# Optimization experiments

Measured on AMD Instinct MI355X. Metric: run time of the kernel, lower is better.

Reference implementation:

```python
import jax, jax.numpy as jnp
import numpy as np

BATCH, SEQ, DIM, HEADS, DSTATE, BLOCK = 2, 4096, 1024, 16, 64, 64
LN_EPS = 1e-6

def segsum(x):
    # x: (..., T) -> (..., T, T); segsum[i, j] = sum_{j < k <= i} x[k]; -inf above diagonal
    T = x.shape[-1]
    cs = jnp.cumsum(x, axis=-1)
    seg = cs[..., :, None] - cs[..., None, :]
    mask = jnp.tril(jnp.ones((T, T), dtype=bool))
    return jnp.where(mask, seg, -jnp.inf)

def ssd_minimal_discrete(X, A, C, B, block_len):
    # X: (b,s,h,p) already multiplied by dt; A: (b,s,h) = A*dt; C readout, B input: (b,s,h,n)
    b, s, h, p = X.shape
    n = B.shape[-1]
    c = s // block_len
    l = block_len
    Xc = X.reshape(b, c, l, h, p)
    Bc = B.reshape(b, c, l, h, n)
    Cc = C.reshape(b, c, l, h, n)
    Ac = A.reshape(b, c, l, h).transpose(0, 3, 1, 2)  # (b,h,c,l)
    A_cumsum = jnp.cumsum(Ac, axis=-1)
    # 1. intra-chunk (diagonal block) outputs
    L = jnp.exp(segsum(Ac))  # (b,h,c,l,l)
    Y_diag = jnp.einsum('bclhn,bcshn,bhcls,bcshp->bclhp', Cc, Bc, L, Xc)
    # 2. states at end of each chunk
    decay_states = jnp.exp(A_cumsum[..., -1:] - A_cumsum)
    states = jnp.einsum('bclhn,bhcl,bclhp->bchpn', Bc, decay_states, Xc)
    # 3. inter-chunk recurrence on chunk states
    init = jnp.zeros_like(states[:, :1])
    states = jnp.concatenate([init, states], axis=1)  # (b,c+1,h,p,n)
    decay_chunk = jnp.exp(segsum(jnp.pad(A_cumsum[..., -1], ((0, 0), (0, 0), (1, 0)))))
    new_states = jnp.einsum('bhzc,bchpn->bzhpn', decay_chunk, states)
    states, final_state = new_states[:, :-1], new_states[:, -1]
    # 4. state -> output contribution (off-diagonal blocks)
    state_decay_out = jnp.exp(A_cumsum)
    Y_off = jnp.einsum('bclhn,bchpn,bhcl->bclhp', Cc, states, state_decay_out)
    return (Y_diag + Y_off).reshape(b, s, h, p), final_state

def setup_inputs():
    key = jax.random.key(0)
    ks = jax.random.split(key, 8)
    X = jax.random.normal(ks[0], (BATCH, SEQ, DIM), jnp.float32)
    B = jax.random.normal(ks[1], (BATCH, SEQ, HEADS * DSTATE), jnp.float32)
    C = jax.random.normal(ks[2], (BATCH, SEQ, HEADS * DSTATE), jnp.float32)
    W_dt = jax.random.normal(ks[3], (DIM, HEADS), jnp.float32) * 0.02
    # dt_bias initializer: inverse-softplus of dt ~ LogUniform(1e-3, 1e-1)
    dt = jnp.exp(jax.random.uniform(ks[4], (1, SEQ, HEADS)) * (jnp.log(0.1) - jnp.log(0.001)) + jnp.log(0.001))
    dt = jnp.clip(dt, 1e-4)
    dt_bias = dt + jnp.log(-jnp.expm1(-dt))
    # a_log initializer: log of Uniform(1, 16)
    a_log = jnp.log(jax.random.uniform(ks[5], (HEADS,), minval=1.0, maxval=16.0))
    W_out = jax.random.normal(ks[6], (DIM, DIM), jnp.float32) * 0.02
    ln_scale = jnp.ones((DIM,), jnp.float32)
    ln_bias = jnp.zeros((DIM,), jnp.float32)
    return {"X": X, "B": B, "C": C, "W_dt": W_dt, "dt_bias": dt_bias, "a_log": a_log,
            "W_out": W_out, "ln_scale": ln_scale, "ln_bias": ln_bias, "block_len": BLOCK}

def reference(X, B, C, W_dt, dt_bias, a_log, W_out, ln_scale, ln_bias, block_len):
    b, s, dim = X.shape
    h = a_log.shape[0]
    Xh = X.reshape(b, s, h, -1)
    Bh = B.reshape(b, s, h, -1)
    Ch = C.reshape(b, s, h, -1)
    dt = jax.nn.softplus(jnp.einsum('bsd,dh->bsh', X, W_dt) + dt_bias)  # (b,s,h)
    A = -jnp.exp(a_log)  # (h,)
    y, final_state = ssd_minimal_discrete(Xh * dt[..., None], A * dt, Ch, Bh, block_len)
    y = y.reshape(b, s, dim)
    mu = jnp.mean(y, axis=-1, keepdims=True)
    var = jnp.mean(jnp.square(y - mu), axis=-1, keepdims=True)
    yn = (y - mu) / jnp.sqrt(var + LN_EPS) * ln_scale + ln_bias
    out = jnp.einsum('bsd,de->bse', yn, W_out)
    return out, final_state
```

## Files before the change

### kernel.cpp

```cpp
#include <hip/hip_runtime.h>
#include <hip/hip_bf16.h>
#include <hip/hip_fp16.h>
#include <math.h>

#define BATCH   2
#define SEQ     4096
#define DIM     1024
#define HEADS   16
#define DSTATE  64
#define HEADDIM 64
#define BLOCKL  64
#define NCHUNK  64
#define ROWS    (BATCH*SEQ)

typedef __attribute__((ext_vector_type(4))) float f32x4;
typedef __attribute__((ext_vector_type(8))) short bf16x8;
typedef __attribute__((ext_vector_type(8))) _Float16 f16x8;

static __device__ __forceinline__ float softplus_f(float x){
    return (x > 20.f) ? x : log1pf(__expf(x));
}
static __device__ __forceinline__ ushort f2b(float f){
    __hip_bfloat16 h = __float2bfloat16(f);
    return *reinterpret_cast<ushort*>(&h);
}
static __device__ __forceinline__ float b2f(ushort u){
    uint x = ((uint)u) << 16;
    return *reinterpret_cast<float*>(&x);
}
static __device__ __forceinline__ void gload16(const void* g, void* l){
    __builtin_amdgcn_global_load_lds((const __attribute__((address_space(1))) unsigned int*)g,
                                     (__attribute__((address_space(3))) unsigned int*)l, 16, 0, 0);
}

__global__ __launch_bounds__(256) void k_dt(const float* __restrict__ X,
        const float* __restrict__ Wdt, const float* __restrict__ dtb,
        const float* __restrict__ alog,
        float* __restrict__ dt_g, float* __restrict__ dtA_g){
    int r = blockIdx.x;
    int s = r & (SEQ-1);
    int tid = threadIdx.x;
    __shared__ float xrow[DIM];
    __shared__ float red[16][17];
    *(f32x4*)(xrow + tid*4) = *(const f32x4*)(X + (size_t)r*DIM + tid*4);
    __syncthreads();
    int part = tid >> 4, h = tid & 15;
    int d0 = part * 64;
    float acc = 0.f;
    #pragma unroll 8
    for (int i = 0; i < 64; ++i)
        acc += xrow[d0 + i] * Wdt[(size_t)(d0 + i)*HEADS + h];
    red[part][h] = acc;
    __syncthreads();
    if (tid < 16){
        float sum = 0.f;
        #pragma unroll
        for (int p = 0; p < 16; ++p) sum += red[p][tid];
        sum += dtb[(size_t)s*HEADS + tid];
        float dtv = softplus_f(sum);
        dt_g[(size_t)r*HEADS + tid]  = dtv;
        dtA_g[(size_t)r*HEADS + tid] = -__expf(alog[tid]) * dtv;
    }
}

__global__ __launch_bounds__(256) void k_chunk(const float* __restrict__ X,
        const float* __restrict__ Bin, const float* __restrict__ Cin,
        const float* __restrict__ dt_g, const float* __restrict__ dtA_g,
        ushort* __restrict__ ybf, ushort* __restrict__ cstate, float* __restrict__ css_g){
    int bid = blockIdx.x;
    int h = bid & 15, c = (bid >> 4) & 63, b = bid >> 10;
    int tid = threadIdx.x;
    int lane = tid & 63, wave = tid >> 6;
    int r0 = b*SEQ + c*BLOCKL;

    __shared__ __align__(16) char region0[18432];
    __shared__ __align__(16) ushort XdT[64*72];
    __shared__ __align__(16) ushort WBT[64*72];
    __shared__ float csh[64], dtsh[64], wsh[64];
    ushort* Cs = (ushort*)region0;
    ushort* Bs = (ushort*)(region0 + 9216);
    float*  Mf = (float*)region0;

    int l  = tid >> 2;
    int c0 = (tid & 3) * 16;

    f32x4 xr[4], br[4], cr[4];
    {
        const float* xp = X   + (size_t)(r0 + l)*DIM + h*HEADDIM + c0;
        const float* bp = Bin + (size_t)(r0 + l)*DIM + h*DSTATE  + c0;
        const float* cp = Cin + (size_t)(r0 + l)*DIM + h*DSTATE  + c0;
        #pragma unroll
        for (int q = 0; q < 4; ++q){
            xr[q] = *(const f32x4*)(xp + q*4);
            br[q] = *(const f32x4*)(bp + q*4);
            cr[q] = *(const f32x4*)(cp + q*4);
        }
    }
    if (tid < 64){
        dtsh[tid] = dt_g[(size_t)(r0 + tid)*HEADS + h];
        float a = dtA_g[(size_t)(r0 + tid)*HEADS + h];
        #pragma unroll
        for (int off = 1; off < 64; off <<= 1){
            float v = __shfl_up(a, off, 64);
            if (tid >= off) a += v;
        }
        csh[tid] = a;
        css_g[(size_t)bid*64 + tid] = a;
        float cs63 = __shfl(a, 63, 64);
        wsh[tid] = __expf(cs63 - a);
    }
    ushort tc[16], tb[16];
    #pragma unroll
    for (int q = 0; q < 4; ++q)
        #pragma unroll
        for (int j = 0; j < 4; ++j){
            tc[q*4+j] = f2b(cr[q][j]);
            tb[q*4+j] = f2b(br[q][j]);
        }
    *(uint4*)&Cs[l*72 + c0]     = *(uint4*)&tc[0];
    *(uint4*)&Cs[l*72 + c0 + 8] = *(uint4*)&tc[8];
    *(uint4*)&Bs[l*72 + c0]     = *(uint4*)&tb[0];
    *(uint4*)&Bs[l*72 + c0 + 8] = *(uint4*)&tb[8];
    __syncthreads();

    {
        float dl = dtsh[l], wl = wsh[l];
        #pragma unroll
        for (int q = 0; q < 4; ++q)
            #pragma unroll
            for (int j = 0; j < 4; ++j){
                int p = c0 + q*4 + j;
                XdT[p*72 + l] = f2b(xr[q][j] * dl);
                WBT[p*72 + l] = f2b(br[q][j] * wl);
            }
    }
    __syncthreads();

    int cl15  = lane & 15;
    int g     = lane >> 4;
    int arow  = wave*16 + cl15;
    int kof   = g * 8;
    int rbase = wave*16 + g*4;

    f32x4 gacc[4];
    #pragma unroll
    for (int j = 0; j < 4; ++j) gacc[j] = (f32x4){0.f,0.f,0.f,0.f};
    #pragma unroll
    for (int k = 0; k < 2; ++k){
        bf16x8 a = *(const bf16x8*)&Cs[arow*72 + k*32 + kof];
        #pragma unroll
        for (int j = 0; j < 4; ++j){
            bf16x8 bb = *(const bf16x8*)&Bs[(16*j + cl15)*72 + k*32 + kof];
            gacc[j] = __builtin_amdgcn_mfma_f32_16x16x32_bf16(a, bb, gacc[j], 0, 0, 0);
        }
    }
    __syncthreads();

    #pragma unroll
    for (int j = 0; j < 4; ++j){
        #pragma unroll
        for (int r = 0; r < 4; ++r){
            int row = rbase + r, col = 16*j + cl15;
            float m = 0.f;
            if (col <= row) m = gacc[j][r] * __expf(csh[row] - csh[col]);
            Mf[row*65 + col] = m;
        }
    }
    __syncthreads();

    f32x4 y[4];
    #pragma unroll
    for (int j = 0; j < 4; ++j) y[j] = (f32x4){0.f,0.f,0.f,0.f};
    #pragma unroll
    for (int k = 0; k < 2; ++k){
        bf16x8 am;
        #pragma unroll
        for (int i = 0; i < 8; ++i)
            am[i] = (short)f2b(Mf[arow*65 + k*32 + kof + i]);
        #pragma unroll
        for (int j = 0; j < 4; ++j){
            bf16x8 bx = *(const bf16x8*)&XdT[(16*j + cl15)*72 + k*32 + kof];
            y[j] = __builtin_amdgcn_mfma_f32_16x16x32_bf16(am, bx, y[j], 0, 0, 0);
        }
    }
    #pragma unroll
    for (int j = 0; j < 4; ++j)
        #pragma unroll
        for (int r = 0; r < 4; ++r)
            ybf[(size_t)(r0 + rbase + r)*DIM + h*HEADDIM + 16*j + cl15] = f2b(y[j][r]);

    f32x4 st[4];
    #pragma unroll
    for (int j = 0; j < 4; ++j) st[j] = (f32x4){0.f,0.f,0.f,0.f};
    #pragma unroll
    for (int k = 0; k < 2; ++k){
        bf16x8 aw = *(const bf16x8*)&XdT[arow*72 + k*32 + kof];
        #pragma unroll
        for (int j = 0; j < 4; ++j){
            bf16x8 bb = *(const bf16x8*)&WBT[(16*j + cl15)*72 + k*32 + kof];
            st[j] = __builtin_amdgcn_mfma_f32_16x16x32_bf16(aw, bb, st[j], 0, 0, 0);
        }
    }
    #pragma unroll
    for (int j = 0; j < 4; ++j)
        #pragma unroll
        for (int r = 0; r < 4; ++r){
            __half hv = __float2half(st[j][r]);
            cstate[(size_t)bid*4096 + (size_t)(rbase + r)*64 + 16*j + cl15] = *(ushort*)&hv;
        }
}

__global__ __launch_bounds__(256) void k_scan(ushort* __restrict__ cstate,
        const float* __restrict__ css_g, float* __restrict__ fs_out){
    int bid = blockIdx.x;
    int tile = bid & 7, hh = (bid >> 3) & 15, b = bid >> 7;
    int pn = tile*512 + threadIdx.x*2;
    float P0 = 0.f, P1 = 0.f;
    for (int c = 0; c < NCHUNK; ++c){
        size_t base = (size_t)((b*NCHUNK + c)*HEADS + hh);
        float e = __expf(css_g[base*64 + 63]);
        __half2 cur = *(const __half2*)&cstate[base*4096 + pn];
        *( __half2*)&cstate[base*4096 + pn] = __floats2half2_rn(P0, P1);
        float2 cf = __half22float2(cur);
        P0 = e*P0 + cf.x;
        P1 = e*P1 + cf.y;
    }
    *(float2*)&fs_out[(size_t)(b*HEADS + hh)*4096 + pn] = make_float2(P0, P1);
}

__global__ __launch_bounds__(256) void k_yoff(const float* __restrict__ Cin,
        const ushort* __restrict__ cstate, const float* __restrict__ css_g,
        ushort* __restrict__ ybf){
    int bid = blockIdx.x;
    int h = bid & 15, c = (bid >> 4) & 63, b = bid >> 10;
    int tid = threadIdx.x;
    int lane = tid & 63, wave = tid >> 6;
    int r0 = b*SEQ + c*BLOCKL;
    __shared__ __align__(16) ushort Cs[64*72];
    __shared__ __align__(16) ushort Ss[64*72];
    __shared__ float cse[64];
    {
        int l  = tid >> 2;
        int c0 = (tid & 3) * 16;
        const float* cp = Cin + (size_t)(r0 + l)*DIM + h*DSTATE + c0;
        ushort tc[16];
        #pragma unroll
        for (int q = 0; q < 4; ++q){
            f32x4 vc = *(const f32x4*)(cp + q*4);
            #pragma unroll
            for (int j = 0; j < 4; ++j){
                __half hv = __float2half(vc[j]);
                tc[q*4+j] = *(ushort*)&hv;
            }
        }
        *(uint4*)&Cs[l*72 + c0]     = *(uint4*)&tc[0];
        *(uint4*)&Cs[l*72 + c0 + 8] = *(uint4*)&tc[8];
        const ushort* sp = cstate + (size_t)bid*4096 + (size_t)l*64 + c0;
        *(uint4*)&Ss[l*72 + c0]     = *(const uint4*)sp;
        *(uint4*)&Ss[l*72 + c0 + 8] = *(const uint4*)(sp + 8);
    }
    if (tid < 64) cse[tid] = __expf(css_g[(size_t)bid*64 + tid]);
    __syncthreads();

    int cl15 = lane & 15;
    int g    = lane >> 4;
    int arow = wave*16 + cl15;
    int kof  = g * 8;
    f32x4 acc[4];
    #pragma unroll
    for (int j = 0; j < 4; ++j) acc[j] = (f32x4){0.f,0.f,0.f,0.f};
    #pragma unroll
    for (int k = 0; k < 2; ++k){
        f16x8 a = *(const f16x8*)&Cs[arow*72 + k*32 + kof];
        #pragma unroll
        for (int j = 0; j < 4; ++j){
            f16x8 bb = *(const f16x8*)&Ss[(16*j + cl15)*72 + k*32 + kof];
            acc[j] = __builtin_amdgcn_mfma_f32_16x16x32_f16(a, bb, acc[j], 0, 0, 0);
        }
    }
    int rbase = wave*16 + g*4;
    #pragma unroll
    for (int j = 0; j < 4; ++j)
        #pragma unroll
        for (int r = 0; r < 4; ++r){
            float e = cse[rbase + r];
            size_t idx = (size_t)(r0 + rbase + r)*DIM + h*HEADDIM + 16*j + cl15;
            ybf[idx] = f2b(b2f(ybf[idx]) + e * acc[j][r]);
        }
}

__global__ __launch_bounds__(256) void k_ln(ushort* __restrict__ ybf,
        const float* __restrict__ scale, const float* __restrict__ bias){
    int r = blockIdx.x, tid = threadIdx.x;
    ushort* yp = ybf + (size_t)r*DIM + tid*4;
    short4 raw = *(const short4*)yp;
    float v[4];
    v[0] = b2f((ushort)raw.x); v[1] = b2f((ushort)raw.y);
    v[2] = b2f((ushort)raw.z); v[3] = b2f((ushort)raw.w);
    float s1 = v[0]+v[1]+v[2]+v[3];
    float s2 = v[0]*v[0]+v[1]*v[1]+v[2]*v[2]+v[3]*v[3];
    #pragma unroll
    for (int m = 32; m > 0; m >>= 1){
        s1 += __shfl_xor(s1, m, 64);
        s2 += __shfl_xor(s2, m, 64);
    }
    __shared__ float w1[4], w2[4];
    int wv = tid >> 6;
    if ((tid & 63) == 0){ w1[wv] = s1; w2[wv] = s2; }
    __syncthreads();
    float S1 = w1[0]+w1[1]+w1[2]+w1[3];
    float S2 = w2[0]+w2[1]+w2[2]+w2[3];
    float mu  = S1 * (1.f/DIM);
    float var = S2 * (1.f/DIM) - mu*mu;
    float rstd = rsqrtf(var + 1e-6f);
    int d = tid*4;
    f32x4 sc = *(const f32x4*)(scale + d);
    f32x4 bi = *(const f32x4*)(bias + d);
    ushort o[4];
    #pragma unroll
    for (int j = 0; j < 4; ++j)
        o[j] = f2b((v[j] - mu)*rstd*sc[j] + bi[j]);
    *(short4*)yp = *(short4*)&o[0];
}

__global__ __launch_bounds__(256) void k_wt(const float* __restrict__ W,
        __hip_bfloat16* __restrict__ Wt){
    __shared__ float t[64][65];
    int kt = blockIdx.x >> 4, nt = blockIdx.x & 15;
    int tid = threadIdx.x;
    int lr = tid >> 4, lc4 = (tid & 15) * 4;
    #pragma unroll
    for (int q = 0; q < 4; ++q){
        int k = lr + q*16;
        *(f32x4*)&t[k][lc4] = *(const f32x4*)(W + (size_t)(kt*64 + k)*DIM + nt*64 + lc4);
    }
    __syncthreads();
    #pragma unroll
    for (int q = 0; q < 4; ++q){
        int n = lr + q*16;
        union { __hip_bfloat16 h[4]; short4 s4; } u;
        #pragma unroll
        for (int j = 0; j < 4; ++j) u.h[j] = __float2bfloat16(t[lc4+j][n]);
        *(short4*)((short*)Wt + (size_t)(nt*64 + n)*DIM + kt*64 + lc4) = u.s4;
    }
}

__global__ __launch_bounds__(256) void k_gemm(const __hip_bfloat16* __restrict__ A,
        const __hip_bfloat16* __restrict__ Bt, float* __restrict__ Out){
    __shared__ __align__(16) ushort As[128*32];
    __shared__ __align__(16) ushort Bsh[128*32];
    int bid = blockIdx.x;
    int bn = bid & 7, bm = bid >> 3;
    int tid = threadIdx.x;
    int lane = tid & 63, wave = tid >> 6;
    int wr = wave >> 1, wc = wave & 1;
    f32x4 acc[4][4];
    #pragma unroll
    for (int i = 0; i < 4; ++i)
        #pragma unroll
        for (int j = 0; j < 4; ++j)
            acc[i][j] = (f32x4){0.f, 0.f, 0.f, 0.f};
    const ushort* Ag = (const ushort*)A  + (size_t)bm*128*1024;
    const ushort* Bg = (const ushort*)Bt + (size_t)bn*128*1024;
    int row0 = tid >> 2;
    int col0 = (tid & 3) * 8;
    for (int k0 = 0; k0 < 1024; k0 += 32){
        const ushort* sA = Ag + (size_t)row0*1024 + k0 + col0;
        const ushort* sB = Bg + (size_t)row0*1024 + k0 + col0;
        gload16(sA,           &As[row0*32 + col0]);
        gload16(sA + 64*1024, &As[(row0+64)*32 + col0]);
        gload16(sB,           &Bsh[row0*32 + col0]);
        gload16(sB + 64*1024, &Bsh[(row0+64)*32 + col0]);
        __syncthreads();
        bf16x8 af[4], bfr[4];
        #pragma unroll
        for (int i = 0; i < 4; ++i){
            int arow = wr*64 + i*16 + (lane & 15);
            af[i] = *(const bf16x8*)&As[arow*32 + ((lane >> 4) << 3)];
        }
        #pragma unroll
        for (int j = 0; j < 4; ++j){
            int brow = wc*64 + j*16 + (lane & 15);
            bfr[j] = *(const bf16x8*)&Bsh[brow*32 + ((lane >> 4) << 3)];
        }
        #pragma unroll
        for (int i = 0; i < 4; ++i)
            #pragma unroll
            for (int j = 0; j < 4; ++j)
                acc[i][j] = __builtin_amdgcn_mfma_f32_16x16x32_bf16(af[i], bfr[j], acc[i][j], 0, 0, 0);
        __syncthreads();
    }
    #pragma unroll
    for (int i = 0; i < 4; ++i){
        int m0 = bm*128 + wr*64 + i*16 + ((lane >> 4) << 2);
        #pragma unroll
        for (int j = 0; j < 4; ++j){
            int n = bn*128 + wc*64 + j*16 + (lane & 15);
            #pragma unroll
            for (int reg = 0; reg < 4; ++reg)
                Out[(size_t)(m0 + reg)*1024 + n] = acc[i][j][reg];
        }
    }
}

extern "C" void kernel_launch(void* const* d_in, const int* in_sizes, int n_in,
                              void* d_out, int out_size, void* d_ws, size_t ws_size,
                              hipStream_t stream){
    const float* X    = (const float*)d_in[0];
    const float* Bin  = (const float*)d_in[1];
    const float* Cin  = (const float*)d_in[2];
    const float* Wdt  = (const float*)d_in[3];
    const float* dtb  = (const float*)d_in[4];
    const float* alog = (const float*)d_in[5];
    const float* Wout = (const float*)d_in[6];
    const float* lns  = (const float*)d_in[7];
    const float* lnb  = (const float*)d_in[8];

    float* out = (float*)d_out;
    float* fs_out = out + (size_t)ROWS*DIM;

    float* dt_g   = (float*)d_ws;
    float* dtA_g  = dt_g  + 131072;
    float* css_g  = dtA_g + 131072;
    ushort* cstate = (ushort*)(css_g + 131072);
    ushort* ybf    = cstate + 8388608;
    __hip_bfloat16* Wt = (__hip_bfloat16*)(ybf + 8388608);

    k_dt   <<<ROWS,               256, 0, stream>>>(X, Wdt, dtb, alog, dt_g, dtA_g);
    k_chunk<<<BATCH*NCHUNK*HEADS, 256, 0, stream>>>(X, Bin, Cin, dt_g, dtA_g, ybf, cstate, css_g);
    k_scan <<<BATCH*HEADS*8,      256, 0, stream>>>(cstate, css_g, fs_out);
    k_yoff <<<BATCH*NCHUNK*HEADS, 256, 0, stream>>>(Cin, cstate, css_g, ybf);
    k_ln   <<<ROWS,               256, 0, stream>>>(ybf, lns, lnb);
    k_wt   <<<256,                256, 0, stream>>>(Wout, Wt);
    k_gemm <<<512,                256, 0, stream>>>((const __hip_bfloat16*)ybf, Wt, out);
}
```

Before: 127.0 us.

## Fuse weight transpose into dt kernel, shrink chunk LDS, prefetch scan, remap GEMM blocks

Merges the W_out transpose/bf16 cast into the dt projection kernel as extra blocks, which removes one launch. In the chunk kernel, the masked score matrix is now stored in LDS as bf16 and read with vector loads, and XdT reuses the C/B region, which shrinks LDS use and may allow more resident blocks. The scan prefetches the next chunk state before it is needed. The GEMM block index is remapped so that consecutive blocks share B tiles, for better cache locality. These are several unrelated tweaks, each with a modest expected effect.

```diff
diff --git a/kernel.cpp b/kernel.cpp
--- a/kernel.cpp
+++ b/kernel.cpp
@@ -33,33 +33,56 @@
                                      (__attribute__((address_space(3))) unsigned int*)l, 16, 0, 0);
 }
 
-__global__ __launch_bounds__(256) void k_dt(const float* __restrict__ X,
+__global__ __launch_bounds__(256) void k_dtwt(const float* __restrict__ X,
         const float* __restrict__ Wdt, const float* __restrict__ dtb,
-        const float* __restrict__ alog,
-        float* __restrict__ dt_g, float* __restrict__ dtA_g){
-    int r = blockIdx.x;
-    int s = r & (SEQ-1);
-    int tid = threadIdx.x;
+        const float* __restrict__ alog, const float* __restrict__ W,
+        float* __restrict__ dt_g, float* __restrict__ dtA_g,
+        ushort* __restrict__ Wt){
     __shared__ float xrow[DIM];
     __shared__ float red[16][17];
-    *(f32x4*)(xrow + tid*4) = *(const f32x4*)(X + (size_t)r*DIM + tid*4);
-    __syncthreads();
-    int part = tid >> 4, h = tid & 15;
-    int d0 = part * 64;
-    float acc = 0.f;
-    #pragma unroll 8
-    for (int i = 0; i < 64; ++i)
-        acc += xrow[d0 + i] * Wdt[(size_t)(d0 + i)*HEADS + h];
-    red[part][h] = acc;
-    __syncthreads();
-    if (tid < 16){
-        float sum = 0.f;
-        #pragma unroll
-        for (int p = 0; p < 16; ++p) sum += red[p][tid];
-        sum += dtb[(size_t)s*HEADS + tid];
-        float dtv = softplus_f(sum);
-        dt_g[(size_t)r*HEADS + tid]  = dtv;
-        dtA_g[(size_t)r*HEADS + tid] = -__expf(alog[tid]) * dtv;
+    __shared__ float t[64][65];
+    int bidx = blockIdx.x;
+    int tid = threadIdx.x;
+    if (bidx < ROWS){
+        int r = bidx;
+        int s = r & (SEQ-1);
+        *(f32x4*)(xrow + tid*4) = *(const f32x4*)(X + (size_t)r*DIM + tid*4);
+        __syncthreads();
+        int part = tid >> 4, h = tid & 15;
+        int d0 = part * 64;
+        float acc = 0.f;
+        #pragma unroll 8
+        for (int i = 0; i < 64; ++i)
+            acc += xrow[d0 + i] * Wdt[(size_t)(d0 + i)*HEADS + h];
+        red[part][h] = acc;
+        __syncthreads();
+        if (tid < 16){
+            float sum = 0.f;
+            #pragma unroll
+            for (int p = 0; p < 16; ++p) sum += red[p][tid];
+            sum += dtb[(size_t)s*HEADS + tid];
+            float dtv = softplus_f(sum);
+            dt_g[(size_t)r*HEADS + tid]  = dtv;
+            dtA_g[(size_t)r*HEADS + tid] = -__expf(alog[tid]) * dtv;
+        }
+    } else {
+        int bid = bidx - ROWS;
+        int kt = bid >> 4, nt = bid & 15;
+        int lr = tid >> 4, lc4 = (tid & 15) * 4;
+        #pragma unroll
+        for (int q = 0; q < 4; ++q){
+            int k = lr + q*16;
+            *(f32x4*)&t[k][lc4] = *(const f32x4*)(W + (size_t)(kt*64 + k)*DIM + nt*64 + lc4);
+        }
+        __syncthreads();
+        #pragma unroll
+        for (int q = 0; q < 4; ++q){
+            int n = lr + q*16;
+            ushort o[4];
+            #pragma unroll
+            for (int j = 0; j < 4; ++j) o[j] = f2b(t[lc4+j][n]);
+            *(short4*)(Wt + (size_t)(nt*64 + n)*DIM + kt*64 + lc4) = *(short4*)&o[0];
+        }
     }
 }
 
@@ -74,12 +97,12 @@
     int r0 = b*SEQ + c*BLOCKL;
 
     __shared__ __align__(16) char region0[18432];
-    __shared__ __align__(16) ushort XdT[64*72];
     __shared__ __align__(16) ushort WBT[64*72];
     __shared__ float csh[64], dtsh[64], wsh[64];
-    ushort* Cs = (ushort*)region0;
-    ushort* Bs = (ushort*)(region0 + 9216);
-    float*  Mf = (float*)region0;
+    ushort* Cs  = (ushort*)region0;
+    ushort* Bs  = (ushort*)(region0 + 9216);
+    ushort* Mb  = (ushort*)region0;
+    ushort* XdT = (ushort*)(region0 + 9216);
 
     int l  = tid >> 2;
     int c0 = (tid & 3) * 16;
@@ -109,30 +132,19 @@
         float cs63 = __shfl(a, 63, 64);
         wsh[tid] = __expf(cs63 - a);
     }
-    ushort tc[16], tb[16];
-    #pragma unroll
-    for (int q = 0; q < 4; ++q)
-        #pragma unroll
-        for (int j = 0; j < 4; ++j){
-            tc[q*4+j] = f2b(cr[q][j]);
-            tb[q*4+j] = f2b(br[q][j]);
-        }
-    *(uint4*)&Cs[l*72 + c0]     = *(uint4*)&tc[0];
-    *(uint4*)&Cs[l*72 + c0 + 8] = *(uint4*)&tc[8];
-    *(uint4*)&Bs[l*72 + c0]     = *(uint4*)&tb[0];
-    *(uint4*)&Bs[l*72 + c0 + 8] = *(uint4*)&tb[8];
-    __syncthreads();
-
     {
-        float dl = dtsh[l], wl = wsh[l];
+        ushort tc[16], tb[16];
         #pragma unroll
         for (int q = 0; q < 4; ++q)
             #pragma unroll
             for (int j = 0; j < 4; ++j){
-                int p = c0 + q*4 + j;
-                XdT[p*72 + l] = f2b(xr[q][j] * dl);
-                WBT[p*72 + l] = f2b(br[q][j] * wl);
+                tc[q*4+j] = f2b(cr[q][j]);
+                tb[q*4+j] = f2b(br[q][j]);
             }
+        *(uint4*)&Cs[l*72 + c0]     = *(uint4*)&tc[0];
+        *(uint4*)&Cs[l*72 + c0 + 8] = *(uint4*)&tc[8];
+        *(uint4*)&Bs[l*72 + c0]     = *(uint4*)&tb[0];
+        *(uint4*)&Bs[l*72 + c0 + 8] = *(uint4*)&tb[8];
     }
     __syncthreads();
 
@@ -142,6 +154,14 @@
     int kof   = g * 8;
     int rbase = wave*16 + g*4;
 
+    {
+        float wl = wsh[l];
+        #pragma unroll
+        for (int q = 0; q < 4; ++q)
+            #pragma unroll
+            for (int j = 0; j < 4; ++j)
+                WBT[(c0 + q*4 + j)*72 + l] = f2b(br[q][j] * wl);
+    }
     f32x4 gacc[4];
     #pragma unroll
     for (int j = 0; j < 4; ++j) gacc[j] = (f32x4){0.f,0.f,0.f,0.f};
@@ -163,8 +183,16 @@
             int row = rbase + r, col = 16*j + cl15;
             float m = 0.f;
             if (col <= row) m = gacc[j][r] * __expf(csh[row] - csh[col]);
-            Mf[row*65 + col] = m;
-        }
+            Mb[row*72 + col] = f2b(m);
+        }
+    }
+    {
+        float dl = dtsh[l];
+        #pragma unroll
+        for (int q = 0; q < 4; ++q)
+            #pragma unroll
+            for (int j = 0; j < 4; ++j)
+                XdT[(c0 + q*4 + j)*72 + l] = f2b(xr[q][j] * dl);
     }
     __syncthreads();
 
@@ -173,10 +201,7 @@
     for (int j = 0; j < 4; ++j) y[j] = (f32x4){0.f,0.f,0.f,0.f};
     #pragma unroll
     for (int k = 0; k < 2; ++k){
-        bf16x8 am;
-        #pragma unroll
-        for (int i = 0; i < 8; ++i)
-            am[i] = (short)f2b(Mf[arow*65 + k*32 + kof + i]);
+        bf16x8 am = *(const bf16x8*)&Mb[arow*72 + k*32 + kof];
         #pragma unroll
         for (int j = 0; j < 4; ++j){
             bf16x8 bx = *(const bf16x8*)&XdT[(16*j + cl15)*72 + k*32 + kof];
@@ -215,15 +240,19 @@
     int bid = blockIdx.x;
     int tile = bid & 7, hh = (bid >> 3) & 15, b = bid >> 7;
     int pn = tile*512 + threadIdx.x*2;
+    size_t base0 = (size_t)(b*NCHUNK)*HEADS + hh;
     float P0 = 0.f, P1 = 0.f;
+    __half2 cur = *(const __half2*)&cstate[base0*4096 + pn];
     for (int c = 0; c < NCHUNK; ++c){
-        size_t base = (size_t)((b*NCHUNK + c)*HEADS + hh);
+        size_t base = base0 + (size_t)c*HEADS;
+        __half2 nxt = cur;
+        if (c < NCHUNK-1) nxt = *(const __half2*)&cstate[(base + HEADS)*4096 + pn];
         float e = __expf(css_g[base*64 + 63]);
-        __half2 cur = *(const __half2*)&cstate[base*4096 + pn];
         *( __half2*)&cstate[base*4096 + pn] = __floats2half2_rn(P0, P1);
         float2 cf = __half22float2(cur);
         P0 = e*P0 + cf.x;
         P1 = e*P1 + cf.y;
+        cur = nxt;
     }
     *(float2*)&fs_out[(size_t)(b*HEADS + hh)*4096 + pn] = make_float2(P0, P1);
 }
@@ -323,34 +352,13 @@
     *(short4*)yp = *(short4*)&o[0];
 }
 
-__global__ __launch_bounds__(256) void k_wt(const float* __restrict__ W,
-        __hip_bfloat16* __restrict__ Wt){
-    __shared__ float t[64][65];
-    int kt = blockIdx.x >> 4, nt = blockIdx.x & 15;
-    int tid = threadIdx.x;
-    int lr = tid >> 4, lc4 = (tid & 15) * 4;
-    #pragma unroll
-    for (int q = 0; q < 4; ++q){
-        int k = lr + q*16;
-        *(f32x4*)&t[k][lc4] = *(const f32x4*)(W + (size_t)(kt*64 + k)*DIM + nt*64 + lc4);
-    }
-    __syncthreads();
-    #pragma unroll
-    for (int q = 0; q < 4; ++q){
-        int n = lr + q*16;
-        union { __hip_bfloat16 h[4]; short4 s4; } u;
-        #pragma unroll
-        for (int j = 0; j < 4; ++j) u.h[j] = __float2bfloat16(t[lc4+j][n]);
-        *(short4*)((short*)Wt + (size_t)(nt*64 + n)*DIM + kt*64 + lc4) = u.s4;
-    }
-}
-
-__global__ __launch_bounds__(256) void k_gemm(const __hip_bfloat16* __restrict__ A,
-        const __hip_bfloat16* __restrict__ Bt, float* __restrict__ Out){
+__global__ __launch_bounds__(256) void k_gemm(const ushort* __restrict__ A,
+        const ushort* __restrict__ Bt, float* __restrict__ Out){
     __shared__ __align__(16) ushort As[128*32];
     __shared__ __align__(16) ushort Bsh[128*32];
     int bid = blockIdx.x;
-    int bn = bid & 7, bm = bid >> 3;
+    int wgid = (bid & 7)*64 + (bid >> 3);
+    int bn = wgid & 7, bm = wgid >> 3;
     int tid = threadIdx.x;
     int lane = tid & 63, wave = tid >> 6;
     int wr = wave >> 1, wc = wave & 1;
@@ -360,8 +368,8 @@
         #pragma unroll
         for (int j = 0; j < 4; ++j)
             acc[i][j] = (f32x4){0.f, 0.f, 0.f, 0.f};
-    const ushort* Ag = (const ushort*)A  + (size_t)bm*128*1024;
-    const ushort* Bg = (const ushort*)Bt + (size_t)bn*128*1024;
+    const ushort* Ag = A  + (size_t)bm*128*1024;
+    const ushort* Bg = Bt + (size_t)bn*128*1024;
     int row0 = tid >> 2;
     int col0 = (tid & 3) * 8;
     for (int k0 = 0; k0 < 1024; k0 += 32){
@@ -419,18 +427,18 @@
     float* out = (float*)d_out;
     float* fs_out = out + (size_t)ROWS*DIM;
 
-    float* dt_g   = (float*)d_ws;
-    float* dtA_g  = dt_g  + 131072;
-    float* css_g  = dtA_g + 131072;
-    ushort* cstate = (ushort*)(css_g + 131072);
-    ushort* ybf    = cstate + 8388608;
-    __hip_bfloat16* Wt = (__hip_bfloat16*)(ybf + 8388608);
-
-    k_dt   <<<ROWS,               256, 0, stream>>>(X, Wdt, dtb, alog, dt_g, dtA_g);
+    char* ws = (char*)d_ws;
+    float*  dt_g   = (float*)(ws);
+    float*  dtA_g  = (float*)(ws + 524288);
+    float*  css_g  = (float*)(ws + 1048576);
+    ushort* cstate = (ushort*)(ws + 1572864);
+    ushort* ybf    = (ushort*)(ws + 18350080);
+    ushort* Wt     = (ushort*)(ws + 35127296);
+
+    k_dtwt <<<ROWS + 256,         256, 0, stream>>>(X, Wdt, dtb, alog, Wout, dt_g, dtA_g, Wt);
     k_chunk<<<BATCH*NCHUNK*HEADS, 256, 0, stream>>>(X, Bin, Cin, dt_g, dtA_g, ybf, cstate, css_g);
     k_scan <<<BATCH*HEADS*8,      256, 0, stream>>>(cstate, css_g, fs_out);
     k_yoff <<<BATCH*NCHUNK*HEADS, 256, 0, stream>>>(Cin, cstate, css_g, ybf);
     k_ln   <<<ROWS,               256, 0, stream>>>(ybf, lns, lnb);
-    k_wt   <<<256,                256, 0, stream>>>(Wout, Wt);
-    k_gemm <<<512,                256, 0, stream>>>((const __hip_bfloat16*)ybf, Wt, out);
-}
+    k_gemm <<<512,                256, 0, stream>>>(ybf, Wt, out);
+}
```

Measured after the change: 123.0 us. 3.1% less time.
